# Optimization experiments

Hardware: AMD Instinct MI355X
Metric: run time of the kernel (lower is better)

## Reference

```python
import jax, jax.numpy as jnp
import numpy as np

B, N, VF = 8, 2048, 11   # batch, nodes per graph, node feature dim
F1, F2 = 32, 64          # EGCN internal filters (projected back to VF)
HEADS = 3


def egcn(x, A, W1, W2, Wo):
    # x: [B,N,VF], A: [B,N,N]. Gather/aggregate messages then gated update.
    m = jnp.einsum('bnm,bmf->bnf', A, x)          # neighbor aggregation (memory-bound)
    h = jnp.tanh((x @ W1) * (m @ W2))             # [B,N,filters]
    return h @ Wo                                  # project back to [B,N,VF]


def self_attention(x, w):
    # x: [B,N,VF], w: [HEADS,VF]; additive attention pooling per head.
    scores = jax.nn.softmax(jnp.tanh(jnp.einsum('bnf,hf->bhn', x, w)), axis=-1)
    rep = jnp.einsum('bhn,bnf->bhf', scores, x).reshape(x.shape[0], -1)  # [B,HEADS*VF]
    return rep, scores


def setup_inputs() -> dict:
    key = jax.random.key(0)
    ks = jax.random.split(key, 16)
    s = 0.1
    return {
        'x_int': jax.random.normal(ks[0], (B, N, VF), jnp.float32),
        'x_nh': jax.random.normal(ks[1], (B, N, VF), jnp.float32),
        'A_int': jax.random.uniform(ks[2], (B, N, N), jnp.float32) / N,
        'A_nh': jax.random.uniform(ks[3], (B, N, N), jnp.float32) / N,
        'conv1_W1': jax.random.normal(ks[4], (VF, F1), jnp.float32) * s,
        'conv1_W2': jax.random.normal(ks[5], (VF, F1), jnp.float32) * s,
        'conv1_Wo': jax.random.normal(ks[6], (F1, VF), jnp.float32) * s,
        'conv2_W1': jax.random.normal(ks[7], (VF, F2), jnp.float32) * s,
        'conv2_W2': jax.random.normal(ks[8], (VF, F2), jnp.float32) * s,
        'conv2_Wo': jax.random.normal(ks[9], (F2, VF), jnp.float32) * s,
        'att_int_w': jax.random.normal(ks[10], (HEADS, VF), jnp.float32) * s,
        'att_nh_w': jax.random.normal(ks[11], (HEADS, VF), jnp.float32) * s,
        'dense_W': jax.random.normal(ks[12], (2 * HEADS * VF, 1), jnp.float32) * s,
        'dense_b': jnp.zeros((1,), jnp.float32),
    }


def reference(x_int, x_nh, A_int, A_nh,
              conv1_W1, conv1_W2, conv1_Wo,
              conv2_W1, conv2_W2, conv2_Wo,
              att_int_w, att_nh_w, dense_W, dense_b):
    # conv1 (shared weights applied to both graphs)
    x_int = egcn(x_int, A_int, conv1_W1, conv1_W2, conv1_Wo)
    x_nh = egcn(x_nh, A_nh, conv1_W1, conv1_W2, conv1_Wo)
    # conv2
    x_int = egcn(x_int, A_int, conv2_W1, conv2_W2, conv2_Wo)
    x_nh = egcn(x_nh, A_nh, conv2_W1, conv2_W2, conv2_Wo)
    # dual self-attention pooling
    r_int, _ = self_attention(x_int, att_int_w)   # [B, 33]
    r_nh, _ = self_attention(x_nh, att_nh_w)      # [B, 33]
    r = jnp.concatenate((r_int, r_nh), axis=1)    # [B, 66]
    out = r @ dense_W + dense_b                   # linear head
    return jnp.squeeze(out, 1)                    # [B]
```

## Files before the change

kernel.cpp:

```cpp
#include <hip/hip_runtime.h>
#include <math.h>

#define NN 2048
#define BB 8
#define VFF 11
#define MSPLIT 4
#define MLEN (NN / MSPLIT)
#define SBUF ((size_t)BB * VFF * NN)

__device__ __forceinline__ float tanh_poly(float z) {
  float t = z * z;
  return z * fmaf(t, fmaf(t, 0.13333334f, -0.33333334f), 1.0f);
}

template <int CTRL>
__device__ __forceinline__ float ror_add(float v) {
  int r = __builtin_amdgcn_update_dpp(0, __float_as_int(v), CTRL, 0xF, 0xF, true);
  return v + __int_as_float(r);
}

__global__ __launch_bounds__(256) void k_transpose(
    const float* __restrict__ x_int, const float* __restrict__ x_nh,
    float* __restrict__ xT_int, float* __restrict__ xT_nh) {
  int idx = blockIdx.x * 256 + threadIdx.x;
  const float* src = blockIdx.y ? x_nh : x_int;
  float* dst = blockIdx.y ? xT_nh : xT_int;
  int b = idx >> 11, n = idx & (NN - 1);
#pragma unroll
  for (int f = 0; f < VFF; ++f)
    dst[(size_t)(b * VFF + f) * NN + n] = src[(size_t)idx * VFF + f];
}

__global__ __launch_bounds__(256, 4) void k_agg(
    const float* __restrict__ A_int, const float* __restrict__ A_nh,
    const float* __restrict__ xT_int, const float* __restrict__ xT_nh,
    float* __restrict__ mP) {
  __shared__ float xs[VFF][MLEN];
  const int tid = threadIdx.x;
  const int wave = tid >> 6, lane = tid & 63;
  const int grp = lane >> 4, ph = lane & 15;
  const int b = blockIdx.y;
  const int g = blockIdx.z >> 2, split = blockIdx.z & (MSPLIT - 1);
  const int rbase = blockIdx.x * 64 + wave * 16;
  const int r0 = rbase + grp * 4;
  const int mbase = split * MLEN;
  const float* A = g ? A_nh : A_int;
  const float* xT = g ? xT_nh : xT_int;
  const float* A0 = A + ((size_t)(b * NN + r0)) * NN + mbase + ph * 4;
  const float* xb = xT + (size_t)b * VFF * NN + mbase;

  for (int i = tid; i < VFF * (MLEN / 4); i += 256) {
    int f = i >> 7, mm = i & 127;
    ((float4*)xs[f])[mm] = ((const float4*)(xb + (size_t)f * NN))[mm];
  }
  __syncthreads();

  float acc0[VFF], acc1[VFF], acc2[VFF], acc3[VFF];
#pragma unroll
  for (int f = 0; f < VFF; ++f) {
    acc0[f] = 0.f; acc1[f] = 0.f; acc2[f] = 0.f; acc3[f] = 0.f;
  }

  for (int m = 0; m < MLEN; m += 64) {
    float4 a0 = *(const float4*)(A0 + m);
    float4 a1 = *(const float4*)(A0 + NN + m);
    float4 a2 = *(const float4*)(A0 + 2 * NN + m);
    float4 a3 = *(const float4*)(A0 + 3 * NN + m);
#pragma unroll
    for (int f = 0; f < VFF; ++f) {
      float4 xv = *(const float4*)(&xs[f][m + ph * 4]);
      acc0[f] = fmaf(a0.x, xv.x, acc0[f]);
      acc0[f] = fmaf(a0.y, xv.y, acc0[f]);
      acc0[f] = fmaf(a0.z, xv.z, acc0[f]);
      acc0[f] = fmaf(a0.w, xv.w, acc0[f]);
      acc1[f] = fmaf(a1.x, xv.x, acc1[f]);
      acc1[f] = fmaf(a1.y, xv.y, acc1[f]);
      acc1[f] = fmaf(a1.z, xv.z, acc1[f]);
      acc1[f] = fmaf(a1.w, xv.w, acc1[f]);
      acc2[f] = fmaf(a2.x, xv.x, acc2[f]);
      acc2[f] = fmaf(a2.y, xv.y, acc2[f]);
      acc2[f] = fmaf(a2.z, xv.z, acc2[f]);
      acc2[f] = fmaf(a2.w, xv.w, acc2[f]);
      acc3[f] = fmaf(a3.x, xv.x, acc3[f]);
      acc3[f] = fmaf(a3.y, xv.y, acc3[f]);
      acc3[f] = fmaf(a3.z, xv.z, acc3[f]);
      acc3[f] = fmaf(a3.w, xv.w, acc3[f]);
    }
  }

#pragma unroll
  for (int f = 0; f < VFF; ++f) {
    float v0 = acc0[f], v1 = acc1[f], v2 = acc2[f], v3 = acc3[f];
    v0 = ror_add<0x128>(v0); v0 = ror_add<0x124>(v0);
    v0 = ror_add<0x122>(v0); v0 = ror_add<0x121>(v0);
    v1 = ror_add<0x128>(v1); v1 = ror_add<0x124>(v1);
    v1 = ror_add<0x122>(v1); v1 = ror_add<0x121>(v1);
    v2 = ror_add<0x128>(v2); v2 = ror_add<0x124>(v2);
    v2 = ror_add<0x122>(v2); v2 = ror_add<0x121>(v2);
    v3 = ror_add<0x128>(v3); v3 = ror_add<0x124>(v3);
    v3 = ror_add<0x122>(v3); v3 = ror_add<0x121>(v3);
    acc0[f] = v0; acc1[f] = v1; acc2[f] = v2; acc3[f] = v3;
  }

  float* outp = mP + (size_t)(g * MSPLIT + split) * SBUF +
                (size_t)b * VFF * NN + r0;
  if (ph == 0) {
#pragma unroll
    for (int f = 0; f < VFF; ++f) outp[f * NN + 0] = acc0[f];
  } else if (ph == 1) {
#pragma unroll
    for (int f = 0; f < VFF; ++f) outp[f * NN + 1] = acc1[f];
  } else if (ph == 2) {
#pragma unroll
    for (int f = 0; f < VFF; ++f) outp[f * NN + 2] = acc2[f];
  } else if (ph == 3) {
#pragma unroll
    for (int f = 0; f < VFF; ++f) outp[f * NN + 3] = acc3[f];
  }
}

template <int F>
__global__ __launch_bounds__(256) void k_pw(
    const float* __restrict__ xT_int, const float* __restrict__ xT_nh,
    const float* __restrict__ mP,
    const float* __restrict__ W1, const float* __restrict__ W2,
    const float* __restrict__ Wo,
    float* __restrict__ yT_int, float* __restrict__ yT_nh) {
  int g = blockIdx.y;
  int idx = blockIdx.x * 256 + threadIdx.x;
  int b = idx >> 11, n = idx & (NN - 1);
  const float* xT = g ? xT_nh : xT_int;
  float* yT = g ? yT_nh : yT_int;
  const float* mp = mP + (size_t)g * MSPLIT * SBUF;
  size_t base = (size_t)b * VFF * NN + n;
  float xv[VFF], mv[VFF], y[VFF];
#pragma unroll
  for (int f = 0; f < VFF; ++f) {
    xv[f] = xT[base + f * NN];
    mv[f] = mp[base + f * NN] + mp[SBUF + base + f * NN] +
            mp[2 * SBUF + base + f * NN] + mp[3 * SBUF + base + f * NN];
    y[f] = 0.f;
  }
#pragma unroll 4
  for (int j = 0; j < F; ++j) {
    float a = 0.f, c = 0.f;
#pragma unroll
    for (int f = 0; f < VFF; ++f) {
      a = fmaf(xv[f], W1[f * F + j], a);
      c = fmaf(mv[f], W2[f * F + j], c);
    }
    float h = tanh_poly(a * c);
#pragma unroll
    for (int f = 0; f < VFF; ++f) y[f] = fmaf(h, Wo[j * VFF + f], y[f]);
  }
#pragma unroll
  for (int f = 0; f < VFF; ++f) yT[base + f * NN] = y[f];
}

__global__ __launch_bounds__(256) void k_attn(
    const float* __restrict__ xT_int, const float* __restrict__ xT_nh,
    const float* __restrict__ w_int, const float* __restrict__ w_nh,
    float* __restrict__ reps) {
  __shared__ float s[NN];
  __shared__ float red[4];
  int tid = threadIdx.x, wave = tid >> 6, lane = tid & 63;
  int b = blockIdx.x, g = blockIdx.y, h = blockIdx.z;
  const float* xT = (g ? xT_nh : xT_int) + (size_t)b * VFF * NN;
  const float* w = (g ? w_nh : w_int) + h * VFF;
  float wv[VFF];
#pragma unroll
  for (int f = 0; f < VFF; ++f) wv[f] = w[f];

  float p = 0.f;
  for (int n = tid; n < NN; n += 256) {
    float d = 0.f;
#pragma unroll
    for (int f = 0; f < VFF; ++f) d = fmaf(xT[f * NN + n], wv[f], d);
    float e = expf(tanh_poly(d));
    s[n] = e;
    p += e;
  }
  for (int off = 32; off; off >>= 1) p += __shfl_xor(p, off);
  if (lane == 0) red[wave] = p;
  __syncthreads();
  float inv = 1.f / (red[0] + red[1] + red[2] + red[3]);

  float* orep = reps + ((size_t)(b * 2 + g) * 3 + h) * VFF;
  for (int f = wave; f < VFF; f += 4) {
    const float* xf = xT + (size_t)f * NN;
    float q = 0.f;
    for (int n = lane; n < NN; n += 64) q = fmaf(s[n], xf[n], q);
    for (int off = 32; off; off >>= 1) q += __shfl_xor(q, off);
    if (lane == 0) orep[f] = q * inv;
  }
}

__global__ __launch_bounds__(64) void k_head(
    const float* __restrict__ reps, const float* __restrict__ dW,
    const float* __restrict__ db, float* __restrict__ out) {
  int t = threadIdx.x;
  if (t < BB) {
    float acc = db[0];
#pragma unroll 2
    for (int k = 0; k < 66; ++k) acc = fmaf(reps[t * 66 + k], dW[k], acc);
    out[t] = acc;
  }
}

extern "C" void kernel_launch(void* const* d_in, const int* in_sizes, int n_in,
                              void* d_out, int out_size, void* d_ws, size_t ws_size,
                              hipStream_t stream) {
  const float* x_int = (const float*)d_in[0];
  const float* x_nh  = (const float*)d_in[1];
  const float* A_int = (const float*)d_in[2];
  const float* A_nh  = (const float*)d_in[3];
  const float* c1W1  = (const float*)d_in[4];
  const float* c1W2  = (const float*)d_in[5];
  const float* c1Wo  = (const float*)d_in[6];
  const float* c2W1  = (const float*)d_in[7];
  const float* c2W2  = (const float*)d_in[8];
  const float* c2Wo  = (const float*)d_in[9];
  const float* awi   = (const float*)d_in[10];
  const float* awn   = (const float*)d_in[11];
  const float* dW    = (const float*)d_in[12];
  const float* db    = (const float*)d_in[13];
  float* out = (float*)d_out;
  float* ws = (float*)d_ws;

  float* xTa_i = ws + 0 * SBUF;
  float* xTb_i = ws + 1 * SBUF;
  float* xTc_i = ws + 2 * SBUF;
  float* xTa_n = ws + 3 * SBUF;
  float* xTb_n = ws + 4 * SBUF;
  float* xTc_n = ws + 5 * SBUF;
  float* mP    = ws + 6 * SBUF;
  float* reps  = ws + (6 + 2 * MSPLIT) * SBUF;

  dim3 gT(BB * NN / 256, 2);
  k_transpose<<<gT, 256, 0, stream>>>(x_int, x_nh, xTa_i, xTa_n);

  dim3 gA(NN / 64, BB, 2 * MSPLIT);
  dim3 gPW(BB * NN / 256, 2);
  k_agg<<<gA, 256, 0, stream>>>(A_int, A_nh, xTa_i, xTa_n, mP);
  k_pw<32><<<gPW, 256, 0, stream>>>(xTa_i, xTa_n, mP, c1W1, c1W2, c1Wo, xTb_i, xTb_n);
  k_agg<<<gA, 256, 0, stream>>>(A_int, A_nh, xTb_i, xTb_n, mP);
  k_pw<64><<<gPW, 256, 0, stream>>>(xTb_i, xTb_n, mP, c2W1, c2W2, c2Wo, xTc_i, xTc_n);

  k_attn<<<dim3(BB, 2, 3), 256, 0, stream>>>(xTc_i, xTc_n, awi, awn, reps);
  k_head<<<1, 64, 0, stream>>>(reps, dW, db, out);
}
```

Baseline: 168.7 us.

## Stream A tiles into LDS with async global_load_lds triple buffering

The aggregation kernel now reads A through per-wave triple-buffered LDS windows filled by direct global-to-LDS loads, prefetching two windows ahead. Before, each thread loaded float4 rows of A straight into registers. The goal is to keep more memory requests in flight and overlap A streaming with the FMA work. In exchange it adds 48KB of LDS per block, lowers the occupancy hint from 4 to 2 blocks, and depends on hand-written vmcnt waits and swizzled addressing being correct.

```diff
diff --git a/kernel.cpp b/kernel.cpp
--- a/kernel.cpp
+++ b/kernel.cpp
@@ -6,6 +6,8 @@
 #define VFF 11
 #define MSPLIT 4
 #define MLEN (NN / MSPLIT)
+#define WCOLS 64
+#define NWIN (MLEN / WCOLS)
 #define SBUF ((size_t)BB * VFF * NN)
 
 __device__ __forceinline__ float tanh_poly(float z) {
@@ -31,11 +33,12 @@
     dst[(size_t)(b * VFF + f) * NN + n] = src[(size_t)idx * VFF + f];
 }
 
-__global__ __launch_bounds__(256, 4) void k_agg(
+__global__ __launch_bounds__(256, 2) void k_agg(
     const float* __restrict__ A_int, const float* __restrict__ A_nh,
     const float* __restrict__ xT_int, const float* __restrict__ xT_nh,
     float* __restrict__ mP) {
   __shared__ float xs[VFF][MLEN];
+  __shared__ __align__(16) unsigned int abuf[4][3][1024];
   const int tid = threadIdx.x;
   const int wave = tid >> 6, lane = tid & 63;
   const int grp = lane >> 4, ph = lane & 15;
@@ -46,7 +49,7 @@
   const int mbase = split * MLEN;
   const float* A = g ? A_nh : A_int;
   const float* xT = g ? xT_nh : xT_int;
-  const float* A0 = A + ((size_t)(b * NN + r0)) * NN + mbase + ph * 4;
+  const float* Aw = A + ((size_t)(b * NN + rbase)) * NN + mbase;
   const float* xb = xT + (size_t)b * VFF * NN + mbase;
 
   for (int i = tid; i < VFF * (MLEN / 4); i += 256) {
@@ -55,20 +58,52 @@
   }
   __syncthreads();
 
+  const float* gbase[4];
+#pragma unroll
+  for (int k = 0; k < 4; ++k) {
+    int row = k * 4 + (lane >> 4);
+    int cc = (lane - k * 4 - (lane >> 4)) & 15;
+    gbase[k] = Aw + (size_t)row * NN + cc * 4;
+  }
+
+#define ISSUE(bufi, wcol)                                                     \
+  {                                                                           \
+    _Pragma("unroll") for (int k = 0; k < 4; ++k)                             \
+        __builtin_amdgcn_global_load_lds(                                     \
+            (const __attribute__((address_space(1))) unsigned int*)(gbase[k] + (wcol)), \
+            (__attribute__((address_space(3))) unsigned int*)&abuf[wave][bufi][k * 256], \
+            16, 0, 0);                                                        \
+  }
+
   float acc0[VFF], acc1[VFF], acc2[VFF], acc3[VFF];
 #pragma unroll
   for (int f = 0; f < VFF; ++f) {
     acc0[f] = 0.f; acc1[f] = 0.f; acc2[f] = 0.f; acc3[f] = 0.f;
   }
 
-  for (int m = 0; m < MLEN; m += 64) {
-    float4 a0 = *(const float4*)(A0 + m);
-    float4 a1 = *(const float4*)(A0 + NN + m);
-    float4 a2 = *(const float4*)(A0 + 2 * NN + m);
-    float4 a3 = *(const float4*)(A0 + 3 * NN + m);
+  ISSUE(0, 0);
+  ISSUE(1, WCOLS);
+
+  int bw = 0;
+  for (int w = 0; w < NWIN; ++w) {
+    if (w < NWIN - 1) {
+      asm volatile("s_waitcnt vmcnt(4)" ::: "memory");
+    } else {
+      asm volatile("s_waitcnt vmcnt(0)" ::: "memory");
+    }
+    __builtin_amdgcn_sched_barrier(0);
+    if (w + 2 < NWIN) {
+      int bn = bw + 2; if (bn >= 3) bn -= 3;
+      ISSUE(bn, (w + 2) * WCOLS);
+    }
+    const unsigned int* bp = abuf[wave][bw];
+    float4 a0 = *(const float4*)&bp[(grp * 4 + 0) * 64 + (((ph + grp * 4 + 0) & 15) * 4)];
+    float4 a1 = *(const float4*)&bp[(grp * 4 + 1) * 64 + (((ph + grp * 4 + 1) & 15) * 4)];
+    float4 a2 = *(const float4*)&bp[(grp * 4 + 2) * 64 + (((ph + grp * 4 + 2) & 15) * 4)];
+    float4 a3 = *(const float4*)&bp[(grp * 4 + 3) * 64 + (((ph + grp * 4 + 3) & 15) * 4)];
 #pragma unroll
     for (int f = 0; f < VFF; ++f) {
-      float4 xv = *(const float4*)(&xs[f][m + ph * 4]);
+      float4 xv = *(const float4*)(&xs[f][w * WCOLS + ph * 4]);
       acc0[f] = fmaf(a0.x, xv.x, acc0[f]);
       acc0[f] = fmaf(a0.y, xv.y, acc0[f]);
       acc0[f] = fmaf(a0.z, xv.z, acc0[f]);
@@ -86,7 +121,9 @@
       acc3[f] = fmaf(a3.z, xv.z, acc3[f]);
       acc3[f] = fmaf(a3.w, xv.w, acc3[f]);
     }
-  }
+    bw = (bw == 2) ? 0 : bw + 1;
+  }
+#undef ISSUE
 
 #pragma unroll
   for (int f = 0; f < VFF; ++f) {
```

Result: slower. 179.5 us (+6.4%).
